# Optimization experiments

Hardware: AMD Instinct MI355X
Metric: run time of the kernel (lower is better)

Reference implementation:

```python
import jax, jax.numpy as jnp
import numpy as np

N_NODES = 100000
D = 128
N_EDGES = 500000
EPS = 1e-05


def setup_inputs() -> dict:
    key = jax.random.key(0)
    k1, k2, k3 = jax.random.split(key, 3)
    embed = jax.random.uniform(k1, (N_NODES, D), dtype=jnp.float32)
    weight = jax.random.uniform(k2, (N_EDGES, 1), dtype=jnp.float32)
    edge_idx = jax.random.randint(k3, (N_EDGES, 2), 0, N_NODES, dtype=jnp.int64)
    return {"embed": embed, "weight": weight, "edge_idx": edge_idx}


def reference(embed, weight, edge_idx):
    # Original math: sigmoid(log((A @ B.T) @ w) + 1e-5)
    # where A = embed[edge_idx[:,0]] (E,d), B = embed[edge_idx[:,1]] (E,d), w (E,1).
    # Reassociate (A @ B.T) @ w == A @ (B.T @ w) to avoid the ExE intermediate.
    A = embed[edge_idx[:, 0]]                 # (E, d) gather
    B = embed[edge_idx[:, 1]]                 # (E, d) gather
    btw = jnp.einsum('ed,eo->do', B, weight)  # (d, 1)  tiny contraction
    score = A @ btw                           # (E, 1)
    return jax.nn.sigmoid(jnp.log(score) + EPS)
```

## Files before the change

### kernel.cpp

```cpp
#include <hip/hip_runtime.h>

#define D 128
#define EPS 1e-5f
#define NBLK 2048

__global__ __launch_bounds__(256) void zero_kernel(
    float4* __restrict__ p, int n4)
{
    const int i = blockIdx.x * blockDim.x + threadIdx.x;
    const int stride = gridDim.x * blockDim.x;
    const float4 z = {0.f, 0.f, 0.f, 0.f};
    for (int k = i; k < n4; k += stride) p[k] = z;
}

__global__ __launch_bounds__(256) void wsum_kernel(
    const float* __restrict__ weight,
    const int* __restrict__ eidx,
    float* __restrict__ wsum,
    int nEdges)
{
    const int e = blockIdx.x * blockDim.x + threadIdx.x;
    if (e < nEdges) {
        const int2 p = reinterpret_cast<const int2*>(eidx)[e];
        unsafeAtomicAdd(&wsum[p.y], weight[e]);
    }
}

__global__ __launch_bounds__(256) void btw_partial_kernel(
    const float* __restrict__ embed,
    const float* __restrict__ wsum,
    float* __restrict__ partialT,
    int nNodes)
{
    __shared__ float sbtw[D];
    const int tid = threadIdx.x;
    for (int i = tid; i < D; i += 256) sbtw[i] = 0.f;
    __syncthreads();

    const int j = tid & 31;
    const int hw  = blockIdx.x * 8 + (tid >> 5);
    const int nhw = gridDim.x * 8;

    float4 a0 = {0.f, 0.f, 0.f, 0.f};
    float4 a1 = {0.f, 0.f, 0.f, 0.f};
    int n = hw;
    for (; n + nhw < nNodes; n += 2 * nhw) {
        const float w0 = wsum[n];
        const float w1 = wsum[n + nhw];
        const float4 v0 = reinterpret_cast<const float4*>(embed + (size_t)n * D)[j];
        const float4 v1 = reinterpret_cast<const float4*>(embed + (size_t)(n + nhw) * D)[j];
        a0.x += w0 * v0.x; a0.y += w0 * v0.y; a0.z += w0 * v0.z; a0.w += w0 * v0.w;
        a1.x += w1 * v1.x; a1.y += w1 * v1.y; a1.z += w1 * v1.z; a1.w += w1 * v1.w;
    }
    if (n < nNodes) {
        const float w0 = wsum[n];
        const float4 v0 = reinterpret_cast<const float4*>(embed + (size_t)n * D)[j];
        a0.x += w0 * v0.x; a0.y += w0 * v0.y; a0.z += w0 * v0.z; a0.w += w0 * v0.w;
    }
    a0.x += a1.x; a0.y += a1.y; a0.z += a1.z; a0.w += a1.w;

    atomicAdd(&sbtw[4 * j + 0], a0.x);
    atomicAdd(&sbtw[4 * j + 1], a0.y);
    atomicAdd(&sbtw[4 * j + 2], a0.z);
    atomicAdd(&sbtw[4 * j + 3], a0.w);
    __syncthreads();
    if (tid < D) partialT[(size_t)tid * NBLK + blockIdx.x] = sbtw[tid];
}

__global__ __launch_bounds__(256) void btw_reduce_kernel(
    const float* __restrict__ partialT,
    float* __restrict__ btw)
{
    __shared__ float red[256];
    const int d = blockIdx.x;
    const int tid = threadIdx.x;
    float s = 0.f;
    const float* row = partialT + (size_t)d * NBLK;
    #pragma unroll
    for (int k = tid; k < NBLK; k += 256) s += row[k];
    red[tid] = s;
    __syncthreads();
    for (int off = 128; off > 0; off >>= 1) {
        if (tid < off) red[tid] += red[tid + off];
        __syncthreads();
    }
    if (tid == 0) btw[d] = red[0];
}

__global__ __launch_bounds__(256) void snode_kernel(
    const float* __restrict__ embed,
    const float* __restrict__ btw,
    float* __restrict__ snode,
    int nNodes)
{
    const int tid = threadIdx.x;
    const int j = tid & 31;
    const float4 bt = reinterpret_cast<const float4*>(btw)[j];
    const int hw  = blockIdx.x * 8 + (tid >> 5);
    const int nhw = gridDim.x * 8;

    int n = hw;
    for (; n + nhw < nNodes; n += 2 * nhw) {
        const float4 v0 = reinterpret_cast<const float4*>(embed + (size_t)n * D)[j];
        const float4 v1 = reinterpret_cast<const float4*>(embed + (size_t)(n + nhw) * D)[j];
        float s0 = v0.x * bt.x + v0.y * bt.y + v0.z * bt.z + v0.w * bt.w;
        float s1 = v1.x * bt.x + v1.y * bt.y + v1.z * bt.z + v1.w * bt.w;
        #pragma unroll
        for (int m = 1; m < 32; m <<= 1) {
            s0 += __shfl_xor(s0, m, 64);
            s1 += __shfl_xor(s1, m, 64);
        }
        if (j == 0) {
            snode[n] = s0;
            snode[n + nhw] = s1;
        }
    }
    if (n < nNodes) {
        const float4 v0 = reinterpret_cast<const float4*>(embed + (size_t)n * D)[j];
        float s0 = v0.x * bt.x + v0.y * bt.y + v0.z * bt.z + v0.w * bt.w;
        #pragma unroll
        for (int m = 1; m < 32; m <<= 1)
            s0 += __shfl_xor(s0, m, 64);
        if (j == 0) snode[n] = s0;
    }
}

__global__ __launch_bounds__(256) void out_kernel(
    const int* __restrict__ eidx,
    const float* __restrict__ snode,
    float* __restrict__ out,
    int nEdges)
{
    const int e = blockIdx.x * blockDim.x + threadIdx.x;
    if (e < nEdges) {
        const int2 p = reinterpret_cast<const int2*>(eidx)[e];
        const float x = logf(snode[p.x]) + EPS;
        out[e] = 1.f / (1.f + expf(-x));
    }
}

extern "C" void kernel_launch(void* const* d_in, const int* in_sizes, int n_in,
                              void* d_out, int out_size, void* d_ws, size_t ws_size,
                              hipStream_t stream) {
    const float* embed  = (const float*)d_in[0];
    const float* weight = (const float*)d_in[1];
    const int*   eidx   = (const int*)d_in[2];
    float* out = (float*)d_out;

    const int nEdges = in_sizes[1];
    const int nNodes = in_sizes[0] / D;

    float* wsum     = (float*)d_ws;
    float* btw      = wsum + nNodes;
    float* snode    = btw + D;
    float* partialT = snode + nNodes;

    const int nZero4 = (nNodes + 3) / 4;
    const int eBlocks = (nEdges + 255) / 256;

    zero_kernel       <<<512,     256, 0, stream>>>((float4*)d_ws, nZero4);
    wsum_kernel       <<<eBlocks, 256, 0, stream>>>(weight, eidx, wsum, nEdges);
    btw_partial_kernel<<<NBLK,    256, 0, stream>>>(embed, wsum, partialT, nNodes);
    btw_reduce_kernel <<<D,       256, 0, stream>>>(partialT, btw);
    snode_kernel      <<<NBLK,    256, 0, stream>>>(embed, btw, snode, nNodes);
    out_kernel        <<<eBlocks, 256, 0, stream>>>(eidx, snode, out, nEdges);
}
```

Measured before the change: 71.19 us.

## Replicate wsum atomics, vectorize edge kernels, unroll node loops, simplify sigmoid-log

Spreads the scatter-add of edge weights across eight replicas of the per-node sum array to reduce atomic contention. The replicas are summed when btw_partial reads them. Both edge kernels now handle two edges per thread with int4/float2 loads, and the node loops are unrolled by four. The output replaces log plus exp sigmoid with an algebraically equivalent s/(s+c). The cost is zeroing and reading eight times the wsum memory.

```diff
diff --git a/kernel.cpp b/kernel.cpp
--- a/kernel.cpp
+++ b/kernel.cpp
@@ -1,8 +1,9 @@
 #include <hip/hip_runtime.h>
 
 #define D 128
+#define NREP 8
+#define NBLK 2048
 #define EPS 1e-5f
-#define NBLK 2048
 
 __global__ __launch_bounds__(256) void zero_kernel(
     float4* __restrict__ p, int n4)
@@ -16,19 +17,25 @@
 __global__ __launch_bounds__(256) void wsum_kernel(
     const float* __restrict__ weight,
     const int* __restrict__ eidx,
-    float* __restrict__ wsum,
-    int nEdges)
-{
-    const int e = blockIdx.x * blockDim.x + threadIdx.x;
-    if (e < nEdges) {
-        const int2 p = reinterpret_cast<const int2*>(eidx)[e];
-        unsafeAtomicAdd(&wsum[p.y], weight[e]);
+    float* __restrict__ wsumR,
+    int nNodes, int nEdges)
+{
+    const int t = blockIdx.x * blockDim.x + threadIdx.x;
+    const int e0 = 2 * t;
+    if (e0 + 1 < nEdges) {
+        const int4  p = reinterpret_cast<const int4*>(eidx)[t];
+        const float2 w = reinterpret_cast<const float2*>(weight)[t];
+        unsafeAtomicAdd(&wsumR[(size_t)( e0      & (NREP-1)) * nNodes + p.y], w.x);
+        unsafeAtomicAdd(&wsumR[(size_t)((e0 + 1) & (NREP-1)) * nNodes + p.w], w.y);
+    } else if (e0 < nEdges) {
+        const int dst = eidx[2 * e0 + 1];
+        unsafeAtomicAdd(&wsumR[(size_t)(e0 & (NREP-1)) * nNodes + dst], weight[e0]);
     }
 }
 
 __global__ __launch_bounds__(256) void btw_partial_kernel(
     const float* __restrict__ embed,
-    const float* __restrict__ wsum,
+    const float* __restrict__ wsumR,
     float* __restrict__ partialT,
     int nNodes)
 {
@@ -37,32 +44,47 @@
     for (int i = tid; i < D; i += 256) sbtw[i] = 0.f;
     __syncthreads();
 
-    const int j = tid & 31;
+    const int j   = tid & 31;
     const int hw  = blockIdx.x * 8 + (tid >> 5);
-    const int nhw = gridDim.x * 8;
-
-    float4 a0 = {0.f, 0.f, 0.f, 0.f};
-    float4 a1 = {0.f, 0.f, 0.f, 0.f};
+    const int nhw = NBLK * 8;
+
+    float4 a0 = {0,0,0,0}, a1 = {0,0,0,0}, a2 = {0,0,0,0}, a3 = {0,0,0,0};
     int n = hw;
-    for (; n + nhw < nNodes; n += 2 * nhw) {
-        const float w0 = wsum[n];
-        const float w1 = wsum[n + nhw];
-        const float4 v0 = reinterpret_cast<const float4*>(embed + (size_t)n * D)[j];
-        const float4 v1 = reinterpret_cast<const float4*>(embed + (size_t)(n + nhw) * D)[j];
-        a0.x += w0 * v0.x; a0.y += w0 * v0.y; a0.z += w0 * v0.z; a0.w += w0 * v0.w;
-        a1.x += w1 * v1.x; a1.y += w1 * v1.y; a1.z += w1 * v1.z; a1.w += w1 * v1.w;
-    }
-    if (n < nNodes) {
-        const float w0 = wsum[n];
-        const float4 v0 = reinterpret_cast<const float4*>(embed + (size_t)n * D)[j];
-        a0.x += w0 * v0.x; a0.y += w0 * v0.y; a0.z += w0 * v0.z; a0.w += w0 * v0.w;
-    }
-    a0.x += a1.x; a0.y += a1.y; a0.z += a1.z; a0.w += a1.w;
-
-    atomicAdd(&sbtw[4 * j + 0], a0.x);
-    atomicAdd(&sbtw[4 * j + 1], a0.y);
-    atomicAdd(&sbtw[4 * j + 2], a0.z);
-    atomicAdd(&sbtw[4 * j + 3], a0.w);
+    for (; n + 3 * nhw < nNodes; n += 4 * nhw) {
+        float w0 = 0.f, w1 = 0.f, w2 = 0.f, w3 = 0.f;
+        #pragma unroll
+        for (int r = 0; r < NREP; ++r) {
+            const float* ws = wsumR + (size_t)r * nNodes;
+            w0 += ws[n];
+            w1 += ws[n + nhw];
+            w2 += ws[n + 2 * nhw];
+            w3 += ws[n + 3 * nhw];
+        }
+        const float4 v0 = reinterpret_cast<const float4*>(embed + (size_t)n * D)[j];
+        const float4 v1 = reinterpret_cast<const float4*>(embed + (size_t)(n +     nhw) * D)[j];
+        const float4 v2 = reinterpret_cast<const float4*>(embed + (size_t)(n + 2 * nhw) * D)[j];
+        const float4 v3 = reinterpret_cast<const float4*>(embed + (size_t)(n + 3 * nhw) * D)[j];
+        a0.x += w0*v0.x; a0.y += w0*v0.y; a0.z += w0*v0.z; a0.w += w0*v0.w;
+        a1.x += w1*v1.x; a1.y += w1*v1.y; a1.z += w1*v1.z; a1.w += w1*v1.w;
+        a2.x += w2*v2.x; a2.y += w2*v2.y; a2.z += w2*v2.z; a2.w += w2*v2.w;
+        a3.x += w3*v3.x; a3.y += w3*v3.y; a3.z += w3*v3.z; a3.w += w3*v3.w;
+    }
+    for (; n < nNodes; n += nhw) {
+        float w0 = 0.f;
+        #pragma unroll
+        for (int r = 0; r < NREP; ++r) w0 += wsumR[(size_t)r * nNodes + n];
+        const float4 v0 = reinterpret_cast<const float4*>(embed + (size_t)n * D)[j];
+        a0.x += w0*v0.x; a0.y += w0*v0.y; a0.z += w0*v0.z; a0.w += w0*v0.w;
+    }
+    a0.x += a1.x + a2.x + a3.x;
+    a0.y += a1.y + a2.y + a3.y;
+    a0.z += a1.z + a2.z + a3.z;
+    a0.w += a1.w + a2.w + a3.w;
+
+    atomicAdd(&sbtw[4*j+0], a0.x);
+    atomicAdd(&sbtw[4*j+1], a0.y);
+    atomicAdd(&sbtw[4*j+2], a0.z);
+    atomicAdd(&sbtw[4*j+3], a0.w);
     __syncthreads();
     if (tid < D) partialT[(size_t)tid * NBLK + blockIdx.x] = sbtw[tid];
 }
@@ -97,30 +119,37 @@
     const int j = tid & 31;
     const float4 bt = reinterpret_cast<const float4*>(btw)[j];
     const int hw  = blockIdx.x * 8 + (tid >> 5);
-    const int nhw = gridDim.x * 8;
+    const int nhw = NBLK * 8;
 
     int n = hw;
-    for (; n + nhw < nNodes; n += 2 * nhw) {
-        const float4 v0 = reinterpret_cast<const float4*>(embed + (size_t)n * D)[j];
-        const float4 v1 = reinterpret_cast<const float4*>(embed + (size_t)(n + nhw) * D)[j];
-        float s0 = v0.x * bt.x + v0.y * bt.y + v0.z * bt.z + v0.w * bt.w;
-        float s1 = v1.x * bt.x + v1.y * bt.y + v1.z * bt.z + v1.w * bt.w;
+    for (; n + 3 * nhw < nNodes; n += 4 * nhw) {
+        const float4 v0 = reinterpret_cast<const float4*>(embed + (size_t)n * D)[j];
+        const float4 v1 = reinterpret_cast<const float4*>(embed + (size_t)(n +     nhw) * D)[j];
+        const float4 v2 = reinterpret_cast<const float4*>(embed + (size_t)(n + 2 * nhw) * D)[j];
+        const float4 v3 = reinterpret_cast<const float4*>(embed + (size_t)(n + 3 * nhw) * D)[j];
+        float s0 = v0.x*bt.x + v0.y*bt.y + v0.z*bt.z + v0.w*bt.w;
+        float s1 = v1.x*bt.x + v1.y*bt.y + v1.z*bt.z + v1.w*bt.w;
+        float s2 = v2.x*bt.x + v2.y*bt.y + v2.z*bt.z + v2.w*bt.w;
+        float s3 = v3.x*bt.x + v3.y*bt.y + v3.z*bt.z + v3.w*bt.w;
         #pragma unroll
         for (int m = 1; m < 32; m <<= 1) {
             s0 += __shfl_xor(s0, m, 64);
             s1 += __shfl_xor(s1, m, 64);
+            s2 += __shfl_xor(s2, m, 64);
+            s3 += __shfl_xor(s3, m, 64);
         }
         if (j == 0) {
-            snode[n] = s0;
-            snode[n + nhw] = s1;
+            snode[n]           = s0;
+            snode[n +     nhw] = s1;
+            snode[n + 2 * nhw] = s2;
+            snode[n + 3 * nhw] = s3;
         }
     }
-    if (n < nNodes) {
-        const float4 v0 = reinterpret_cast<const float4*>(embed + (size_t)n * D)[j];
-        float s0 = v0.x * bt.x + v0.y * bt.y + v0.z * bt.z + v0.w * bt.w;
-        #pragma unroll
-        for (int m = 1; m < 32; m <<= 1)
-            s0 += __shfl_xor(s0, m, 64);
+    for (; n < nNodes; n += nhw) {
+        const float4 v0 = reinterpret_cast<const float4*>(embed + (size_t)n * D)[j];
+        float s0 = v0.x*bt.x + v0.y*bt.y + v0.z*bt.z + v0.w*bt.w;
+        #pragma unroll
+        for (int m = 1; m < 32; m <<= 1) s0 += __shfl_xor(s0, m, 64);
         if (j == 0) snode[n] = s0;
     }
 }
@@ -131,11 +160,18 @@
     float* __restrict__ out,
     int nEdges)
 {
-    const int e = blockIdx.x * blockDim.x + threadIdx.x;
-    if (e < nEdges) {
-        const int2 p = reinterpret_cast<const int2*>(eidx)[e];
-        const float x = logf(snode[p.x]) + EPS;
-        out[e] = 1.f / (1.f + expf(-x));
+    const float c = 0.9999900000499999f;
+    const int t = blockIdx.x * blockDim.x + threadIdx.x;
+    const int e0 = 2 * t;
+    if (e0 + 1 < nEdges) {
+        const int4 p = reinterpret_cast<const int4*>(eidx)[t];
+        const float sa = snode[p.x];
+        const float sb = snode[p.z];
+        float2 o = { sa / (sa + c), sb / (sb + c) };
+        reinterpret_cast<float2*>(out)[t] = o;
+    } else if (e0 < nEdges) {
+        const float s = snode[eidx[2 * e0]];
+        out[e0] = s / (s + c);
     }
 }
 
@@ -150,18 +186,18 @@
     const int nEdges = in_sizes[1];
     const int nNodes = in_sizes[0] / D;
 
-    float* wsum     = (float*)d_ws;
-    float* btw      = wsum + nNodes;
+    float* wsumR    = (float*)d_ws;
+    float* btw      = wsumR + (size_t)NREP * nNodes;
     float* snode    = btw + D;
     float* partialT = snode + nNodes;
 
-    const int nZero4 = (nNodes + 3) / 4;
-    const int eBlocks = (nEdges + 255) / 256;
+    const int nZero4  = (NREP * nNodes + 3) / 4;
+    const int pBlocks = ((nEdges + 1) / 2 + 255) / 256;
 
     zero_kernel       <<<512,     256, 0, stream>>>((float4*)d_ws, nZero4);
-    wsum_kernel       <<<eBlocks, 256, 0, stream>>>(weight, eidx, wsum, nEdges);
-    btw_partial_kernel<<<NBLK,    256, 0, stream>>>(embed, wsum, partialT, nNodes);
+    wsum_kernel       <<<pBlocks, 256, 0, stream>>>(weight, eidx, wsumR, nNodes, nEdges);
+    btw_partial_kernel<<<NBLK,    256, 0, stream>>>(embed, wsumR, partialT, nNodes);
     btw_reduce_kernel <<<D,       256, 0, stream>>>(partialT, btw);
     snode_kernel      <<<NBLK,    256, 0, stream>>>(embed, btw, snode, nNodes);
-    out_kernel        <<<eBlocks, 256, 0, stream>>>(eidx, snode, out, nEdges);
-}
+    out_kernel        <<<pBlocks, 256, 0, stream>>>(eidx, snode, out, nEdges);
+}
```

Result: slower. 74.38 us (+4.5%).
